# Performance work log

Measured on AMD Instinct MI355X. Metric: run time of the kernel, lower is better.

## Reference

```python
import jax, jax.numpy as jnp
import numpy as np

N_ENT = 50000
N_EDGE = 500000
D = 256          # ent_hidden_size
H1, C1 = 8, 64   # conv1: heads=8, out=64, concat -> 512
NEG_SLOPE = 0.2
LN_EPS = 1e-5


def setup_inputs() -> dict:
    key = jax.random.key(0)
    ks = jax.random.split(key, 12)
    s = 0.05  # small init scale for numerical sanity
    return {
        "edge_index": jax.random.randint(ks[0], (2, N_EDGE), 0, N_ENT),
        "x": jax.random.normal(ks[1], (N_ENT, D), dtype=jnp.float32),
        "ln_w": jnp.ones((D,), jnp.float32),
        "ln_b": jnp.zeros((D,), jnp.float32),
        "W1": jax.random.normal(ks[2], (D, H1 * C1), dtype=jnp.float32) * s,
        "att_src1": jax.random.normal(ks[3], (H1, C1), dtype=jnp.float32) * s,
        "att_dst1": jax.random.normal(ks[4], (H1, C1), dtype=jnp.float32) * s,
        "b1": jnp.zeros((H1 * C1,), jnp.float32),
        "W2": jax.random.normal(ks[5], (H1 * C1, D), dtype=jnp.float32) * s,
        "att_src2": jax.random.normal(ks[6], (1, D), dtype=jnp.float32) * s,
        "att_dst2": jax.random.normal(ks[7], (1, D), dtype=jnp.float32) * s,
        "b2": jnp.zeros((D,), jnp.float32),
    }


def _gat_conv(x, edge_index, W, att_src, att_dst, bias, heads, out_ch, concat):
    """PyG GATConv (shared src/dst lin, add_self_loops=True, eval-mode dropout)."""
    n = x.shape[0]
    loops = jnp.arange(n)
    src = jnp.concatenate([edge_index[0], loops])  # [E+N]
    dst = jnp.concatenate([edge_index[1], loops])

    h = (x @ W).reshape(n, heads, out_ch)                 # [N,H,C]
    a_src = jnp.sum(h * att_src[None], axis=-1)           # [N,H]
    a_dst = jnp.sum(h * att_dst[None], axis=-1)           # [N,H]

    e = jax.nn.leaky_relu(a_src[src] + a_dst[dst], NEG_SLOPE)  # [E+N,H]
    # per-destination segment softmax (every dst has a self-loop -> no empties)
    m = jax.lax.stop_gradient(jax.ops.segment_max(e, dst, num_segments=n))
    p = jnp.exp(e - m[dst])
    denom = jax.ops.segment_sum(p, dst, num_segments=n)
    alpha = p / denom[dst]                                # [E+N,H]

    out = jax.ops.segment_sum(h[src] * alpha[..., None], dst, num_segments=n)  # [N,H,C]
    out = out.reshape(n, heads * out_ch) if concat else out.mean(axis=1)
    return out + bias


def reference(edge_index, x, ln_w, ln_b, W1, att_src1, att_dst1, b1,
              W2, att_src2, att_dst2, b2):
    # LayerNorm(ent_hidden), eps=1e-5; dropouts are eval-mode no-ops
    mu = jnp.mean(x, axis=-1, keepdims=True)
    var = jnp.var(x, axis=-1, keepdims=True)
    h = (x - mu) / jnp.sqrt(var + LN_EPS) * ln_w + ln_b
    h = jax.nn.elu(_gat_conv(h, edge_index, W1, att_src1, att_dst1, b1, H1, C1, True))
    return _gat_conv(h, edge_index, W2, att_src2, att_dst2, b2, 1, D, False)
```

## Files before the change

kernel.cpp:

```cpp
#include <hip/hip_runtime.h>
#include <hip/hip_bf16.h>
#include <cstdint>

#define N_ENT  50000
#define N_EDGE 500000
#define D_IN   256
constexpr int ETOT = N_EDGE + N_ENT;

typedef __attribute__((ext_vector_type(8))) short bfrag;
typedef __attribute__((ext_vector_type(4))) float f4acc;
typedef __attribute__((ext_vector_type(4))) float f32x4;
typedef __attribute__((ext_vector_type(8))) short s16x8;

__device__ __forceinline__ float lrelu(float x) { return x > 0.f ? x : 0.2f * x; }
__device__ __forceinline__ float eluf(float x)  { return x > 0.f ? x : (expf(x) - 1.f); }
__device__ __forceinline__ short to_bf16(float f) {
    __hip_bfloat16 b = __float2bfloat16(f);
    return *(short*)&b;
}
__device__ __forceinline__ float2 bf2_to_f32(unsigned int u) {
    float2 r;
    r.x = __uint_as_float(u << 16);
    r.y = __uint_as_float(u & 0xffff0000u);
    return r;
}

__global__ __launch_bounds__(256) void prep_kernel(const float* __restrict__ x,
        const float* __restrict__ lnw, const float* __restrict__ lnb,
        short* __restrict__ y, const int* __restrict__ ei, int* __restrict__ cnt,
        const float* __restrict__ W1, short* __restrict__ W1T,
        const float* __restrict__ W2, short* __restrict__ W2T)
{
    int blk = blockIdx.x;
    if (blk < 12500) {
        int n = blk * 4 + (threadIdx.x >> 6);
        int lane = threadIdx.x & 63;
        const f32x4 v = __builtin_nontemporal_load((const f32x4*)(x + (size_t)n * D_IN + lane * 4));
        float s  = v.x + v.y + v.z + v.w;
        float sq = v.x*v.x + v.y*v.y + v.z*v.z + v.w*v.w;
        #pragma unroll
        for (int off = 1; off < 64; off <<= 1) {
            s  += __shfl_xor(s, off);
            sq += __shfl_xor(sq, off);
        }
        float mean = s * (1.f / 256.f);
        float var  = sq * (1.f / 256.f) - mean * mean;
        float rstd = rsqrtf(var + 1e-5f);
        float4 wv = *(const float4*)(lnw + lane * 4);
        float4 bv = *(const float4*)(lnb + lane * 4);
        short4 o;
        o.x = to_bf16((v.x - mean) * rstd * wv.x + bv.x);
        o.y = to_bf16((v.y - mean) * rstd * wv.y + bv.y);
        o.z = to_bf16((v.z - mean) * rstd * wv.z + bv.z);
        o.w = to_bf16((v.w - mean) * rstd * wv.w + bv.w);
        *(short4*)(y + (size_t)n * D_IN + lane * 4) = o;
    } else if (blk < 14454) {
        int e = (blk - 12500) * 256 + threadIdx.x;
        if (e < N_EDGE) atomicAdd(&cnt[ei[N_EDGE + e]], 1);
    } else if (blk < 14966) {
        int i = (blk - 14454) * 256 + threadIdx.x;
        int r = i >> 9, c = i & 511;
        W1T[c * 256 + r] = to_bf16(W1[i]);
    } else {
        int i = (blk - 14966) * 256 + threadIdx.x;
        int r = i >> 8, c = i & 255;
        W2T[c * 512 + r] = to_bf16(W2[i]);
    }
}

template<int NN, int KK, int CH, bool DO_FILL>
__global__ __launch_bounds__(256) void gemm_mfma(const short* __restrict__ A,
        const short* __restrict__ BT, short* __restrict__ C,
        const float* __restrict__ att_s, const float* __restrict__ att_d,
        float* __restrict__ a_s, float* __restrict__ a_d, int M, int nGemm,
        const int* __restrict__ ei, const int* __restrict__ row_start,
        int* __restrict__ cursor2, int* __restrict__ csr_src)
{
    constexpr int GX = NN / 128;
    __shared__ short As[128 * 32];
    __shared__ short Bs[128 * 32];

    if (DO_FILL && (int)blockIdx.x >= nGemm) {
        int e = ((int)blockIdx.x - nGemm) * 256 + threadIdx.x;
        if (e < N_EDGE) {
            int d = ei[N_EDGE + e];
            int pos = atomicAdd(&cursor2[d], 1);
            csr_src[row_start[d] + pos] = ei[e];
        }
        return;
    }

    const int tid  = threadIdx.x;
    const int w    = tid >> 6;
    const int l    = tid & 63;
    const int wm   = w >> 1, wn = w & 1;
    const int m0   = ((int)blockIdx.x / GX) * 128;
    const int n0   = ((int)blockIdx.x % GX) * 128;
    const int quad = l >> 4;
    const int ln16 = l & 15;
    const int rl   = l >> 2;
    const int cs   = l & 3;

    f4acc acc[4][4];
    #pragma unroll
    for (int i = 0; i < 4; ++i)
        #pragma unroll
        for (int j = 0; j < 4; ++j)
            acc[i][j] = (f4acc){0.f, 0.f, 0.f, 0.f};

    for (int k0 = 0; k0 < KK; k0 += 32) {
        __syncthreads();
        #pragma unroll
        for (int tt = 0; tt < 2; ++tt) {
            int t   = w * 2 + tt;
            int row = t * 16 + rl;
            int ca  = cs ^ ((row >> 1) & 3);
            const short* ga = A + (size_t)(m0 + row) * KK + k0 + ca * 8;
            __builtin_amdgcn_global_load_lds(
                (const __attribute__((address_space(1))) unsigned int*)ga,
                (__attribute__((address_space(3))) unsigned int*)&As[t * 512], 16, 0, 0);
            const short* gb = BT + (size_t)(n0 + row) * KK + k0 + ca * 8;
            __builtin_amdgcn_global_load_lds(
                (const __attribute__((address_space(1))) unsigned int*)gb,
                (__attribute__((address_space(3))) unsigned int*)&Bs[t * 512], 16, 0, 0);
        }
        __syncthreads();
        bfrag af[4], bf[4];
        #pragma unroll
        for (int i = 0; i < 4; ++i) {
            int r = wm * 64 + i * 16 + ln16;
            af[i] = *(const bfrag*)&As[r * 32 + (quad ^ ((r >> 1) & 3)) * 8];
            int rn = wn * 64 + i * 16 + ln16;
            bf[i] = *(const bfrag*)&Bs[rn * 32 + (quad ^ ((rn >> 1) & 3)) * 8];
        }
        #pragma unroll
        for (int i = 0; i < 4; ++i)
            #pragma unroll
            for (int j = 0; j < 4; ++j)
                acc[i][j] = __builtin_amdgcn_mfma_f32_16x16x32_bf16(af[i], bf[j], acc[i][j], 0, 0, 0);
    }

    float as_c[4], ad_c[4];
    if constexpr (CH > 0) {
        #pragma unroll
        for (int j = 0; j < 4; ++j) {
            int gc = n0 + wn * 64 + j * 16 + ln16;
            as_c[j] = att_s[gc];
            ad_c[j] = att_d[gc];
        }
    }
    const int hh = (n0 + wn * 64) >> 6;

    #pragma unroll
    for (int i = 0; i < 4; ++i) {
        #pragma unroll
        for (int p = 0; p < 4; ++p) {
            int gr = m0 + wm * 64 + i * 16 + quad * 4 + p;
            float ps = 0.f, pd = 0.f;
            if constexpr (CH > 0) {
                #pragma unroll
                for (int j = 0; j < 4; ++j) {
                    float c = acc[i][j][p];
                    ps = fmaf(c, as_c[j], ps);
                    pd = fmaf(c, ad_c[j], pd);
                }
                #pragma unroll
                for (int off = 1; off < 16; off <<= 1) {
                    ps += __shfl_xor(ps, off);
                    pd += __shfl_xor(pd, off);
                }
            }
            if (gr < M) {
                #pragma unroll
                for (int j = 0; j < 4; ++j) {
                    int gc = n0 + wn * 64 + j * 16 + ln16;
                    C[(size_t)gr * NN + gc] = to_bf16(acc[i][j][p]);
                }
                if constexpr (CH == 64) {
                    if (ln16 == 0) {
                        a_s[(size_t)gr * (NN / 64) + hh] = ps;
                        a_d[(size_t)gr * (NN / 64) + hh] = pd;
                    }
                } else if constexpr (CH == 256) {
                    if (ln16 == 0) {
                        unsafeAtomicAdd(&a_s[gr], ps);
                        unsafeAtomicAdd(&a_d[gr], pd);
                    }
                }
            }
        }
    }
}

__global__ __launch_bounds__(256) void alloc_kernel(const int* __restrict__ cnt,
        int* __restrict__ row_start, int* __restrict__ cursor)
{
    int d = blockIdx.x * 256 + threadIdx.x;
    int lane = threadIdx.x & 63;
    int c = (d < N_ENT) ? cnt[d] : 0;
    int inc = c;
    #pragma unroll
    for (int off = 1; off < 64; off <<= 1) {
        int nb = __shfl_up(inc, off);
        if (lane >= off) inc += nb;
    }
    int waveTotal = __shfl(inc, 63);
    int base = 0;
    if (lane == 63) base = atomicAdd(cursor, waveTotal);
    base = __shfl(base, 63);
    if (d < N_ENT) row_start[d] = base + inc - c;
}

__global__ __launch_bounds__(256) void aggr1_kernel(const int* __restrict__ csr_src,
        const int* __restrict__ row_start, const int* __restrict__ cnt,
        const short* __restrict__ feat, const float* __restrict__ a_s,
        const float* __restrict__ a_d, const float* __restrict__ bias,
        short* __restrict__ out)
{
    int d = blockIdx.x * 4 + (threadIdx.x >> 6);
    if (d >= N_ENT) return;
    int lane = threadIdx.x & 63;
    int f0 = lane * 8;
    int h = lane >> 3;
    int rs = row_start[d];
    int n = cnt[d];
    float adh = a_d[d * 8 + h];

    float den = 0.f;
    float acc[8] = {0.f, 0.f, 0.f, 0.f, 0.f, 0.f, 0.f, 0.f};
    {
        float p = __expf(lrelu(a_s[d * 8 + h] + adh));
        den += p;
        uint4 rv = *(const uint4*)(feat + (size_t)d * 512 + f0);
        float2 t0 = bf2_to_f32(rv.x), t1 = bf2_to_f32(rv.y);
        float2 t2 = bf2_to_f32(rv.z), t3 = bf2_to_f32(rv.w);
        acc[0] += p * t0.x; acc[1] += p * t0.y; acc[2] += p * t1.x; acc[3] += p * t1.y;
        acc[4] += p * t2.x; acc[5] += p * t2.y; acc[6] += p * t3.x; acc[7] += p * t3.y;
    }
    int i = 0;
    for (; i + 4 <= n; i += 4) {
        int   sv[4];
        float ev[4];
        uint4 rv[4];
        #pragma unroll
        for (int u = 0; u < 4; ++u) sv[u] = csr_src[rs + i + u];
        #pragma unroll
        for (int u = 0; u < 4; ++u) ev[u] = a_s[sv[u] * 8 + h];
        #pragma unroll
        for (int u = 0; u < 4; ++u) rv[u] = *(const uint4*)(feat + (size_t)sv[u] * 512 + f0);
        #pragma unroll
        for (int u = 0; u < 4; ++u) {
            float p = __expf(lrelu(ev[u] + adh));
            den += p;
            float2 t0 = bf2_to_f32(rv[u].x), t1 = bf2_to_f32(rv[u].y);
            float2 t2 = bf2_to_f32(rv[u].z), t3 = bf2_to_f32(rv[u].w);
            acc[0] += p * t0.x; acc[1] += p * t0.y; acc[2] += p * t1.x; acc[3] += p * t1.y;
            acc[4] += p * t2.x; acc[5] += p * t2.y; acc[6] += p * t3.x; acc[7] += p * t3.y;
        }
    }
    for (; i < n; ++i) {
        int s = csr_src[rs + i];
        float p = __expf(lrelu(a_s[s * 8 + h] + adh));
        den += p;
        uint4 rv = *(const uint4*)(feat + (size_t)s * 512 + f0);
        float2 t0 = bf2_to_f32(rv.x), t1 = bf2_to_f32(rv.y);
        float2 t2 = bf2_to_f32(rv.z), t3 = bf2_to_f32(rv.w);
        acc[0] += p * t0.x; acc[1] += p * t0.y; acc[2] += p * t1.x; acc[3] += p * t1.y;
        acc[4] += p * t2.x; acc[5] += p * t2.y; acc[6] += p * t3.x; acc[7] += p * t3.y;
    }
    float inv = 1.f / den;
    float4 b0 = *(const float4*)(bias + f0);
    float4 b1 = *(const float4*)(bias + f0 + 4);
    s16x8 o;
    o[0] = to_bf16(eluf(acc[0] * inv + b0.x)); o[1] = to_bf16(eluf(acc[1] * inv + b0.y));
    o[2] = to_bf16(eluf(acc[2] * inv + b0.z)); o[3] = to_bf16(eluf(acc[3] * inv + b0.w));
    o[4] = to_bf16(eluf(acc[4] * inv + b1.x)); o[5] = to_bf16(eluf(acc[5] * inv + b1.y));
    o[6] = to_bf16(eluf(acc[6] * inv + b1.z)); o[7] = to_bf16(eluf(acc[7] * inv + b1.w));
    __builtin_nontemporal_store(o, (s16x8*)(out + (size_t)d * 512 + f0));
}

__global__ __launch_bounds__(256) void aggr2_kernel(const int* __restrict__ csr_src,
        const int* __restrict__ row_start, const int* __restrict__ cnt,
        const short* __restrict__ feat, const float* __restrict__ a_s,
        const float* __restrict__ a_d, const float* __restrict__ bias,
        float* __restrict__ out)
{
    int d = blockIdx.x * 4 + (threadIdx.x >> 6);
    if (d >= N_ENT) return;
    int lane = threadIdx.x & 63;
    int half = lane >> 5;
    int li   = lane & 31;
    int f0   = li * 8;
    int rs = row_start[d];
    int n = cnt[d];
    float adh = a_d[d];

    float den = 0.f;
    float acc[8] = {0.f, 0.f, 0.f, 0.f, 0.f, 0.f, 0.f, 0.f};
    {
        float p = (half == 0) ? __expf(lrelu(a_s[d] + adh)) : 0.f;
        uint4 rv = *(const uint4*)(feat + (size_t)d * 256 + f0);
        den += p;
        float2 t0 = bf2_to_f32(rv.x), t1 = bf2_to_f32(rv.y);
        float2 t2 = bf2_to_f32(rv.z), t3 = bf2_to_f32(rv.w);
        acc[0] += p * t0.x; acc[1] += p * t0.y; acc[2] += p * t1.x; acc[3] += p * t1.y;
        acc[4] += p * t2.x; acc[5] += p * t2.y; acc[6] += p * t3.x; acc[7] += p * t3.y;
    }
    int i = 0;
    for (; i + 4 <= n; i += 4) {
        int e0 = i + half, e1 = i + 2 + half;
        int s0 = csr_src[rs + e0];
        int s1 = csr_src[rs + e1];
        float a0 = a_s[s0], a1 = a_s[s1];
        uint4 rv0 = *(const uint4*)(feat + (size_t)s0 * 256 + f0);
        uint4 rv1 = *(const uint4*)(feat + (size_t)s1 * 256 + f0);
        float p0 = __expf(lrelu(a0 + adh));
        float p1 = __expf(lrelu(a1 + adh));
        den += p0 + p1;
        float2 t0, t1, t2, t3;
        t0 = bf2_to_f32(rv0.x); t1 = bf2_to_f32(rv0.y); t2 = bf2_to_f32(rv0.z); t3 = bf2_to_f32(rv0.w);
        acc[0] += p0 * t0.x; acc[1] += p0 * t0.y; acc[2] += p0 * t1.x; acc[3] += p0 * t1.y;
        acc[4] += p0 * t2.x; acc[5] += p0 * t2.y; acc[6] += p0 * t3.x; acc[7] += p0 * t3.y;
        t0 = bf2_to_f32(rv1.x); t1 = bf2_to_f32(rv1.y); t2 = bf2_to_f32(rv1.z); t3 = bf2_to_f32(rv1.w);
        acc[0] += p1 * t0.x; acc[1] += p1 * t0.y; acc[2] += p1 * t1.x; acc[3] += p1 * t1.y;
        acc[4] += p1 * t2.x; acc[5] += p1 * t2.y; acc[6] += p1 * t3.x; acc[7] += p1 * t3.y;
    }
    for (; i < n; i += 2) {
        int e = i + half;
        bool valid = e < n;
        int s = valid ? csr_src[rs + e] : d;
        float av = a_s[s];
        uint4 rv = *(const uint4*)(feat + (size_t)s * 256 + f0);
        float p = valid ? __expf(lrelu(av + adh)) : 0.f;
        den += p;
        float2 t0 = bf2_to_f32(rv.x), t1 = bf2_to_f32(rv.y);
        float2 t2 = bf2_to_f32(rv.z), t3 = bf2_to_f32(rv.w);
        acc[0] += p * t0.x; acc[1] += p * t0.y; acc[2] += p * t1.x; acc[3] += p * t1.y;
        acc[4] += p * t2.x; acc[5] += p * t2.y; acc[6] += p * t3.x; acc[7] += p * t3.y;
    }
    den += __shfl_xor(den, 32);
    #pragma unroll
    for (int k = 0; k < 8; ++k) acc[k] += __shfl_xor(acc[k], 32);

    float inv = 1.f / den;
    if (half == 0) {
        float4 b0 = *(const float4*)(bias + f0);
        float4 b1 = *(const float4*)(bias + f0 + 4);
        f32x4 o0, o1;
        o0.x = acc[0] * inv + b0.x; o0.y = acc[1] * inv + b0.y;
        o0.z = acc[2] * inv + b0.z; o0.w = acc[3] * inv + b0.w;
        o1.x = acc[4] * inv + b1.x; o1.y = acc[5] * inv + b1.y;
        o1.z = acc[6] * inv + b1.z; o1.w = acc[7] * inv + b1.w;
        __builtin_nontemporal_store(o0, (f32x4*)(out + (size_t)d * 256 + f0));
        __builtin_nontemporal_store(o1, (f32x4*)(out + (size_t)d * 256 + f0 + 4));
    }
}

extern "C" void kernel_launch(void* const* d_in, const int* in_sizes, int n_in,
                              void* d_out, int out_size, void* d_ws, size_t ws_size,
                              hipStream_t stream)
{
    const int*   ei     = (const int*)  d_in[0];
    const float* x      = (const float*)d_in[1];
    const float* ln_w   = (const float*)d_in[2];
    const float* ln_b   = (const float*)d_in[3];
    const float* W1     = (const float*)d_in[4];
    const float* att_s1 = (const float*)d_in[5];
    const float* att_d1 = (const float*)d_in[6];
    const float* b1     = (const float*)d_in[7];
    const float* W2     = (const float*)d_in[8];
    const float* att_s2 = (const float*)d_in[9];
    const float* att_d2 = (const float*)d_in[10];
    const float* b2     = (const float*)d_in[11];
    float* out = (float*)d_out;

    short* h0b = (short*)d_ws;
    short* h1b = h0b + 12800000;
    short* h2b = h1b + 25600000;
    short* h3b = h2b + 25600000;
    short* W1T = h3b + 12800000;
    short* W2T = W1T + 131072;
    float* a_s1 = (float*)(W2T + 131072);
    float* a_d1 = a_s1 + 400000;
    float* a_s2 = a_d1 + 400000;
    float* a_d2 = a_s2 + 50000;
    int* cnt       = (int*)(a_d2 + 50000);
    int* cursor2   = cnt + 50000;
    int* cursor    = cursor2 + 50000;
    int* row_start = cursor + 1;
    int* csr_src   = row_start + 50000;

    hipMemsetAsync(a_s2, 0, 200001 * 4, stream);

    prep_kernel<<<15478, 256, 0, stream>>>(x, ln_w, ln_b, h0b, ei, cnt, W1, W1T, W2, W2T);
    alloc_kernel<<<196, 256, 0, stream>>>(cnt, row_start, cursor);

    constexpr int NG1 = 391 * 4;
    gemm_mfma<512, 256, 64, true><<<NG1 + 1954, 256, 0, stream>>>(
        h0b, W1T, h1b, att_s1, att_d1, a_s1, a_d1, N_ENT, NG1,
        ei, row_start, cursor2, csr_src);
    aggr1_kernel<<<12500, 256, 0, stream>>>(csr_src, row_start, cnt, h1b, a_s1, a_d1, b1, h2b);

    constexpr int NG2 = 391 * 2;
    gemm_mfma<256, 512, 256, false><<<NG2, 256, 0, stream>>>(
        h2b, W2T, h3b, att_s2, att_d2, a_s2, a_d2, N_ENT, NG2,
        nullptr, nullptr, nullptr, nullptr);
    aggr2_kernel<<<12500, 256, 0, stream>>>(csr_src, row_start, cnt, h3b, a_s2, a_d2, b2, out);
}
```

Before: 388.2 us.

## Partition CSR neighbor lists by source half to improve gather locality

During CSR construction, each destination's neighbor list is split into sources below and above a fixed node index. Both aggregation kernels then walk the low-source edges before the high-source edges. The aim is to concentrate the random feature gathers on one half of the feature table at a time and so raise L2/MALL hit rates. This adds a second atomic counter array and extra atomics in the count and fill phases. The aggregation loops get an extra range split, which adds tail iterations.

After: 399.6 us. 2.9% more time.

```diff
diff --git a/kernel.cpp b/kernel.cpp
--- a/kernel.cpp
+++ b/kernel.cpp
@@ -5,6 +5,7 @@
 #define N_ENT  50000
 #define N_EDGE 500000
 #define D_IN   256
+#define SPLIT  25000
 constexpr int ETOT = N_EDGE + N_ENT;
 
 typedef __attribute__((ext_vector_type(8))) short bfrag;
@@ -28,6 +29,7 @@
 __global__ __launch_bounds__(256) void prep_kernel(const float* __restrict__ x,
         const float* __restrict__ lnw, const float* __restrict__ lnb,
         short* __restrict__ y, const int* __restrict__ ei, int* __restrict__ cnt,
+        int* __restrict__ cnt_lo,
         const float* __restrict__ W1, short* __restrict__ W1T,
         const float* __restrict__ W2, short* __restrict__ W2T)
 {
@@ -56,7 +58,12 @@
         *(short4*)(y + (size_t)n * D_IN + lane * 4) = o;
     } else if (blk < 14454) {
         int e = (blk - 12500) * 256 + threadIdx.x;
-        if (e < N_EDGE) atomicAdd(&cnt[ei[N_EDGE + e]], 1);
+        if (e < N_EDGE) {
+            int s = ei[e];
+            int d = ei[N_EDGE + e];
+            atomicAdd(&cnt[d], 1);
+            if (s < SPLIT) atomicAdd(&cnt_lo[d], 1);
+        }
     } else if (blk < 14966) {
         int i = (blk - 14454) * 256 + threadIdx.x;
         int r = i >> 9, c = i & 511;
@@ -74,7 +81,8 @@
         const float* __restrict__ att_s, const float* __restrict__ att_d,
         float* __restrict__ a_s, float* __restrict__ a_d, int M, int nGemm,
         const int* __restrict__ ei, const int* __restrict__ row_start,
-        int* __restrict__ cursor2, int* __restrict__ csr_src)
+        const int* __restrict__ cnt_lo, int* __restrict__ cur_lo,
+        int* __restrict__ cur_hi, int* __restrict__ csr_src)
 {
     constexpr int GX = NN / 128;
     __shared__ short As[128 * 32];
@@ -83,9 +91,16 @@
     if (DO_FILL && (int)blockIdx.x >= nGemm) {
         int e = ((int)blockIdx.x - nGemm) * 256 + threadIdx.x;
         if (e < N_EDGE) {
+            int s = ei[e];
             int d = ei[N_EDGE + e];
-            int pos = atomicAdd(&cursor2[d], 1);
-            csr_src[row_start[d] + pos] = ei[e];
+            int base = row_start[d];
+            if (s < SPLIT) {
+                int pos = atomicAdd(&cur_lo[d], 1);
+                csr_src[base + pos] = s;
+            } else {
+                int pos = atomicAdd(&cur_hi[d], 1);
+                csr_src[base + cnt_lo[d] + pos] = s;
+            }
         }
         return;
     }
@@ -211,8 +226,46 @@
     if (d < N_ENT) row_start[d] = base + inc - c;
 }
 
+__device__ __forceinline__ void aggr1_range(const int* __restrict__ csr_src, int rs,
+        int lo, int hi, const short* __restrict__ feat, const float* __restrict__ a_s,
+        int h, float adh, int f0, float& den, float acc[8])
+{
+    int i = lo;
+    for (; i + 4 <= hi; i += 4) {
+        int   sv[4];
+        float ev[4];
+        uint4 rv[4];
+        #pragma unroll
+        for (int u = 0; u < 4; ++u) sv[u] = csr_src[rs + i + u];
+        #pragma unroll
+        for (int u = 0; u < 4; ++u) ev[u] = a_s[sv[u] * 8 + h];
+        #pragma unroll
+        for (int u = 0; u < 4; ++u) rv[u] = *(const uint4*)(feat + (size_t)sv[u] * 512 + f0);
+        #pragma unroll
+        for (int u = 0; u < 4; ++u) {
+            float p = __expf(lrelu(ev[u] + adh));
+            den += p;
+            float2 t0 = bf2_to_f32(rv[u].x), t1 = bf2_to_f32(rv[u].y);
+            float2 t2 = bf2_to_f32(rv[u].z), t3 = bf2_to_f32(rv[u].w);
+            acc[0] += p * t0.x; acc[1] += p * t0.y; acc[2] += p * t1.x; acc[3] += p * t1.y;
+            acc[4] += p * t2.x; acc[5] += p * t2.y; acc[6] += p * t3.x; acc[7] += p * t3.y;
+        }
+    }
+    for (; i < hi; ++i) {
+        int s = csr_src[rs + i];
+        float p = __expf(lrelu(a_s[s * 8 + h] + adh));
+        den += p;
+        uint4 rv = *(const uint4*)(feat + (size_t)s * 512 + f0);
+        float2 t0 = bf2_to_f32(rv.x), t1 = bf2_to_f32(rv.y);
+        float2 t2 = bf2_to_f32(rv.z), t3 = bf2_to_f32(rv.w);
+        acc[0] += p * t0.x; acc[1] += p * t0.y; acc[2] += p * t1.x; acc[3] += p * t1.y;
+        acc[4] += p * t2.x; acc[5] += p * t2.y; acc[6] += p * t3.x; acc[7] += p * t3.y;
+    }
+}
+
 __global__ __launch_bounds__(256) void aggr1_kernel(const int* __restrict__ csr_src,
         const int* __restrict__ row_start, const int* __restrict__ cnt,
+        const int* __restrict__ cnt_lo,
         const short* __restrict__ feat, const float* __restrict__ a_s,
         const float* __restrict__ a_d, const float* __restrict__ bias,
         short* __restrict__ out)
@@ -224,6 +277,7 @@
     int h = lane >> 3;
     int rs = row_start[d];
     int n = cnt[d];
+    int nLo = cnt_lo[d];
     float adh = a_d[d * 8 + h];
 
     float den = 0.f;
@@ -237,37 +291,9 @@
         acc[0] += p * t0.x; acc[1] += p * t0.y; acc[2] += p * t1.x; acc[3] += p * t1.y;
         acc[4] += p * t2.x; acc[5] += p * t2.y; acc[6] += p * t3.x; acc[7] += p * t3.y;
     }
-    int i = 0;
-    for (; i + 4 <= n; i += 4) {
-        int   sv[4];
-        float ev[4];
-        uint4 rv[4];
-        #pragma unroll
-        for (int u = 0; u < 4; ++u) sv[u] = csr_src[rs + i + u];
-        #pragma unroll
-        for (int u = 0; u < 4; ++u) ev[u] = a_s[sv[u] * 8 + h];
-        #pragma unroll
-        for (int u = 0; u < 4; ++u) rv[u] = *(const uint4*)(feat + (size_t)sv[u] * 512 + f0);
-        #pragma unroll
-        for (int u = 0; u < 4; ++u) {
-            float p = __expf(lrelu(ev[u] + adh));
-            den += p;
-            float2 t0 = bf2_to_f32(rv[u].x), t1 = bf2_to_f32(rv[u].y);
-            float2 t2 = bf2_to_f32(rv[u].z), t3 = bf2_to_f32(rv[u].w);
-            acc[0] += p * t0.x; acc[1] += p * t0.y; acc[2] += p * t1.x; acc[3] += p * t1.y;
-            acc[4] += p * t2.x; acc[5] += p * t2.y; acc[6] += p * t3.x; acc[7] += p * t3.y;
-        }
-    }
-    for (; i < n; ++i) {
-        int s = csr_src[rs + i];
-        float p = __expf(lrelu(a_s[s * 8 + h] + adh));
-        den += p;
-        uint4 rv = *(const uint4*)(feat + (size_t)s * 512 + f0);
-        float2 t0 = bf2_to_f32(rv.x), t1 = bf2_to_f32(rv.y);
-        float2 t2 = bf2_to_f32(rv.z), t3 = bf2_to_f32(rv.w);
-        acc[0] += p * t0.x; acc[1] += p * t0.y; acc[2] += p * t1.x; acc[3] += p * t1.y;
-        acc[4] += p * t2.x; acc[5] += p * t2.y; acc[6] += p * t3.x; acc[7] += p * t3.y;
-    }
+    aggr1_range(csr_src, rs, 0, nLo, feat, a_s, h, adh, f0, den, acc);
+    aggr1_range(csr_src, rs, nLo, n, feat, a_s, h, adh, f0, den, acc);
+
     float inv = 1.f / den;
     float4 b0 = *(const float4*)(bias + f0);
     float4 b1 = *(const float4*)(bias + f0 + 4);
@@ -279,8 +305,59 @@
     __builtin_nontemporal_store(o, (s16x8*)(out + (size_t)d * 512 + f0));
 }
 
+__device__ __forceinline__ void aggr2_range(const int* __restrict__ csr_src, int rs,
+        int lo, int hi, const short* __restrict__ feat, const float* __restrict__ a_s,
+        float adh, int f0, int half, float& den, float acc[8])
+{
+    int i = lo;
+    for (; i + 8 <= hi; i += 8) {
+        int   sv[4];
+        float av[4];
+        uint4 rv[4];
+        #pragma unroll
+        for (int u = 0; u < 4; ++u) sv[u] = csr_src[rs + i + 2 * u + half];
+        #pragma unroll
+        for (int u = 0; u < 4; ++u) av[u] = a_s[sv[u]];
+        #pragma unroll
+        for (int u = 0; u < 4; ++u) rv[u] = *(const uint4*)(feat + (size_t)sv[u] * 256 + f0);
+        #pragma unroll
+        for (int u = 0; u < 4; ++u) {
+            float p = __expf(lrelu(av[u] + adh));
+            den += p;
+            float2 t0 = bf2_to_f32(rv[u].x), t1 = bf2_to_f32(rv[u].y);
+            float2 t2 = bf2_to_f32(rv[u].z), t3 = bf2_to_f32(rv[u].w);
+            acc[0] += p * t0.x; acc[1] += p * t0.y; acc[2] += p * t1.x; acc[3] += p * t1.y;
+            acc[4] += p * t2.x; acc[5] += p * t2.y; acc[6] += p * t3.x; acc[7] += p * t3.y;
+        }
+    }
+    for (; i + 2 <= hi; i += 2) {
+        int s = csr_src[rs + i + half];
+        float av = a_s[s];
+        uint4 rv = *(const uint4*)(feat + (size_t)s * 256 + f0);
+        float p = __expf(lrelu(av + adh));
+        den += p;
+        float2 t0 = bf2_to_f32(rv.x), t1 = bf2_to_f32(rv.y);
+        float2 t2 = bf2_to_f32(rv.z), t3 = bf2_to_f32(rv.w);
+        acc[0] += p * t0.x; acc[1] += p * t0.y; acc[2] += p * t1.x; acc[3] += p * t1.y;
+        acc[4] += p * t2.x; acc[5] += p * t2.y; acc[6] += p * t3.x; acc[7] += p * t3.y;
+    }
+    if (i < hi) {
+        bool valid = (half == 0);
+        int s = valid ? csr_src[rs + i] : 0;
+        float av = a_s[s];
+        uint4 rv = *(const uint4*)(feat + (size_t)s * 256 + f0);
+        float p = valid ? __expf(lrelu(av + adh)) : 0.f;
+        den += p;
+        float2 t0 = bf2_to_f32(rv.x), t1 = bf2_to_f32(rv.y);
+        float2 t2 = bf2_to_f32(rv.z), t3 = bf2_to_f32(rv.w);
+        acc[0] += p * t0.x; acc[1] += p * t0.y; acc[2] += p * t1.x; acc[3] += p * t1.y;
+        acc[4] += p * t2.x; acc[5] += p * t2.y; acc[6] += p * t3.x; acc[7] += p * t3.y;
+    }
+}
+
 __global__ __launch_bounds__(256) void aggr2_kernel(const int* __restrict__ csr_src,
         const int* __restrict__ row_start, const int* __restrict__ cnt,
+        const int* __restrict__ cnt_lo,
         const short* __restrict__ feat, const float* __restrict__ a_s,
         const float* __restrict__ a_d, const float* __restrict__ bias,
         float* __restrict__ out)
@@ -293,6 +370,7 @@
     int f0   = li * 8;
     int rs = row_start[d];
     int n = cnt[d];
+    int nLo = cnt_lo[d];
     float adh = a_d[d];
 
     float den = 0.f;
@@ -306,38 +384,9 @@
         acc[0] += p * t0.x; acc[1] += p * t0.y; acc[2] += p * t1.x; acc[3] += p * t1.y;
         acc[4] += p * t2.x; acc[5] += p * t2.y; acc[6] += p * t3.x; acc[7] += p * t3.y;
     }
-    int i = 0;
-    for (; i + 4 <= n; i += 4) {
-        int e0 = i + half, e1 = i + 2 + half;
-        int s0 = csr_src[rs + e0];
-        int s1 = csr_src[rs + e1];
-        float a0 = a_s[s0], a1 = a_s[s1];
-        uint4 rv0 = *(const uint4*)(feat + (size_t)s0 * 256 + f0);
-        uint4 rv1 = *(const uint4*)(feat + (size_t)s1 * 256 + f0);
-        float p0 = __expf(lrelu(a0 + adh));
-        float p1 = __expf(lrelu(a1 + adh));
-        den += p0 + p1;
-        float2 t0, t1, t2, t3;
-        t0 = bf2_to_f32(rv0.x); t1 = bf2_to_f32(rv0.y); t2 = bf2_to_f32(rv0.z); t3 = bf2_to_f32(rv0.w);
-        acc[0] += p0 * t0.x; acc[1] += p0 * t0.y; acc[2] += p0 * t1.x; acc[3] += p0 * t1.y;
-        acc[4] += p0 * t2.x; acc[5] += p0 * t2.y; acc[6] += p0 * t3.x; acc[7] += p0 * t3.y;
-        t0 = bf2_to_f32(rv1.x); t1 = bf2_to_f32(rv1.y); t2 = bf2_to_f32(rv1.z); t3 = bf2_to_f32(rv1.w);
-        acc[0] += p1 * t0.x; acc[1] += p1 * t0.y; acc[2] += p1 * t1.x; acc[3] += p1 * t1.y;
-        acc[4] += p1 * t2.x; acc[5] += p1 * t2.y; acc[6] += p1 * t3.x; acc[7] += p1 * t3.y;
-    }
-    for (; i < n; i += 2) {
-        int e = i + half;
-        bool valid = e < n;
-        int s = valid ? csr_src[rs + e] : d;
-        float av = a_s[s];
-        uint4 rv = *(const uint4*)(feat + (size_t)s * 256 + f0);
-        float p = valid ? __expf(lrelu(av + adh)) : 0.f;
-        den += p;
-        float2 t0 = bf2_to_f32(rv.x), t1 = bf2_to_f32(rv.y);
-        float2 t2 = bf2_to_f32(rv.z), t3 = bf2_to_f32(rv.w);
-        acc[0] += p * t0.x; acc[1] += p * t0.y; acc[2] += p * t1.x; acc[3] += p * t1.y;
-        acc[4] += p * t2.x; acc[5] += p * t2.y; acc[6] += p * t3.x; acc[7] += p * t3.y;
-    }
+    aggr2_range(csr_src, rs, 0, nLo, feat, a_s, adh, f0, half, den, acc);
+    aggr2_range(csr_src, rs, nLo, n, feat, a_s, adh, f0, half, den, acc);
+
     den += __shfl_xor(den, 32);
     #pragma unroll
     for (int k = 0; k < 8; ++k) acc[k] += __shfl_xor(acc[k], 32);
@@ -384,26 +433,31 @@
     float* a_d1 = a_s1 + 400000;
     float* a_s2 = a_d1 + 400000;
     float* a_d2 = a_s2 + 50000;
-    int* cnt       = (int*)(a_d2 + 50000);
-    int* cursor2   = cnt + 50000;
-    int* cursor    = cursor2 + 50000;
+    int* cnt     = (int*)(a_d2 + 50000);
+    int* cnt_lo  = cnt + 50000;
+    int* cur_lo  = cnt_lo + 50000;
+    int* cur_hi  = cur_lo + 50000;
+    int* cursor  = cur_hi + 50000;
     int* row_start = cursor + 1;
     int* csr_src   = row_start + 50000;
 
-    hipMemsetAsync(a_s2, 0, 200001 * 4, stream);
-
-    prep_kernel<<<15478, 256, 0, stream>>>(x, ln_w, ln_b, h0b, ei, cnt, W1, W1T, W2, W2T);
+    hipMemsetAsync(a_s2, 0, 300001 * 4, stream);
+
+    prep_kernel<<<15478, 256, 0, stream>>>(x, ln_w, ln_b, h0b, ei, cnt, cnt_lo,
+                                           W1, W1T, W2, W2T);
     alloc_kernel<<<196, 256, 0, stream>>>(cnt, row_start, cursor);
 
     constexpr int NG1 = 391 * 4;
     gemm_mfma<512, 256, 64, true><<<NG1 + 1954, 256, 0, stream>>>(
         h0b, W1T, h1b, att_s1, att_d1, a_s1, a_d1, N_ENT, NG1,
-        ei, row_start, cursor2, csr_src);
-    aggr1_kernel<<<12500, 256, 0, stream>>>(csr_src, row_start, cnt, h1b, a_s1, a_d1, b1, h2b);
+        ei, row_start, cnt_lo, cur_lo, cur_hi, csr_src);
+    aggr1_kernel<<<12500, 256, 0, stream>>>(csr_src, row_start, cnt, cnt_lo,
+                                            h1b, a_s1, a_d1, b1, h2b);
 
     constexpr int NG2 = 391 * 2;
     gemm_mfma<256, 512, 256, false><<<NG2, 256, 0, stream>>>(
         h2b, W2T, h3b, att_s2, att_d2, a_s2, a_d2, N_ENT, NG2,
-        nullptr, nullptr, nullptr, nullptr);
-    aggr2_kernel<<<12500, 256, 0, stream>>>(csr_src, row_start, cnt, h3b, a_s2, a_d2, b2, out);
-}
+        nullptr, nullptr, nullptr, nullptr, nullptr, nullptr);
+    aggr2_kernel<<<12500, 256, 0, stream>>>(csr_src, row_start, cnt, cnt_lo,
+                                            h3b, a_s2, a_d2, b2, out);
+}
```
